# Kernel optimization log

Hardware: AMD Instinct MI355X
Metric: run time of the kernel (lower is better)

## Reference

```python
import jax, jax.numpy as jnp
import numpy as np

N_QUBITS = 4
N_LAYERS = 2


def _apply_rx(state, theta, wire):
    """Apply RX(theta) on `wire`. state: [B] + [2]*n complex. theta: [B] or scalar."""
    n = state.ndim - 1
    ax = wire + 1
    half = jnp.asarray(theta) * 0.5
    c = jnp.cos(half)
    s = jnp.sin(half)
    # broadcast angle over the remaining qubit axes after taking the wire slice
    c = jnp.reshape(c, c.shape + (1,) * (n - 1))
    s = jnp.reshape(s, s.shape + (1,) * (n - 1))
    s0 = jnp.take(state, 0, axis=ax)
    s1 = jnp.take(state, 1, axis=ax)
    new0 = c * s0 - 1j * s * s1
    new1 = -1j * s * s0 + c * s1
    return jnp.stack([new0, new1], axis=ax)


def _apply_cnot(state, control, target):
    cax = control + 1
    tax = target + 1
    sub0 = jnp.take(state, 0, axis=cax)
    sub1 = jnp.take(state, 1, axis=cax)
    tax_sub = tax if tax < cax else tax - 1
    sub1 = jnp.flip(sub1, axis=tax_sub)  # X on target when control == 1
    return jnp.stack([sub0, sub1], axis=cax)


def _quantum_circuit(x, w):
    """AngleEmbedding(RX) + BasicEntanglerLayers(RX + CNOT ring), PauliZ expvals.
    x: [B, n_qubits] float32 angles; w: [n_layers, n_qubits] float32.
    Returns [B, n_qubits] float32."""
    B = x.shape[0]
    n = N_QUBITS
    state = jnp.zeros((B,) + (2,) * n, dtype=jnp.complex64)
    state = state.at[(slice(None),) + (0,) * n].set(1.0)
    # AngleEmbedding: RX(x_q) on wire q (per-sample angles)
    for q in range(n):
        state = _apply_rx(state, x[:, q], q)
    # BasicEntanglerLayers: per layer, RX(w[l,q]) on each wire then CNOT ring
    for l in range(N_LAYERS):
        for q in range(n):
            state = _apply_rx(state, w[l, q], q)
        for q in range(n):
            state = _apply_cnot(state, q, (q + 1) % n)
    probs = jnp.abs(state) ** 2  # [B, 2,2,2,2]
    flat = probs.reshape(B, -1)  # [B, 16]
    # <Z_q> = sum_b p(b) * (+1 if bit q == 0 else -1)
    bits = ((jnp.arange(2 ** n)[:, None] >> (n - 1 - jnp.arange(n))[None, :]) & 1)
    signs = (1.0 - 2.0 * bits).astype(jnp.float32)  # [16, n]
    return flat @ signs  # [B, n]


def setup_inputs() -> dict:
    key = jax.random.key(0)
    ks = jax.random.split(key, 5)
    B = 65536
    inputs = jax.random.normal(ks[0], (B, 28, 28), dtype=jnp.float32)
    W1 = jax.random.normal(ks[1], (784, N_QUBITS), dtype=jnp.float32) * 0.05
    b1 = jnp.zeros((N_QUBITS,), dtype=jnp.float32)
    qw = jax.random.normal(ks[2], (N_LAYERS, N_QUBITS), dtype=jnp.float32) * 0.1
    W2 = jax.random.normal(ks[3], (N_QUBITS, 32), dtype=jnp.float32) * 0.3
    b2 = jnp.zeros((32,), dtype=jnp.float32)
    W3 = jax.random.normal(ks[4], (32, 2), dtype=jnp.float32) * 0.2
    b3 = jnp.zeros((2,), dtype=jnp.float32)
    return {"inputs": inputs, "W1": W1, "b1": b1, "qw": qw, "W2": W2, "b2": b2, "W3": W3, "b3": b3}


def reference(inputs, W1, b1, qw, W2, b2, W3, b3):
    B = inputs.shape[0]
    flat = inputs.reshape(B, -1)                      # flatten
    pre = jax.nn.relu(flat @ W1 + b1)                 # dense_preprocess [B, 4]
    q = _quantum_circuit(pre, qw)                     # [B, 4]
    q = jnp.where(jnp.isnan(q), jnp.zeros_like(q), q)
    post = jax.nn.relu(q @ W2 + b2)                   # dense_postprocess [B, 32]
    return jax.nn.softmax(post @ W3 + b3, axis=-1)    # output_layer [B, 2]
```

## Files before the change

### kernel.cpp

```cpp
#include <hip/hip_runtime.h>
#include <math.h>


constexpr int ROW   = 784;
constexpr int ROW4  = 196;
constexpr int CHS   = 20;

__global__ __launch_bounds__(256) void gemv_pre_kernel(
    const float* __restrict__ X,
    const float* __restrict__ W1,
    const float* __restrict__ b1,
    float* __restrict__ pre,
    int B)
{
    __shared__ float w_lds[ROW4 * CHS];

    for (int g = threadIdx.x; g < ROW; g += 256) {
        float4 v = reinterpret_cast<const float4*>(W1)[g];
        int chunk = g >> 2, part = g & 3;
        *reinterpret_cast<float4*>(&w_lds[chunk * CHS + part * 4]) = v;
    }
    const float bi0 = b1[0], bi1 = b1[1], bi2 = b1[2], bi3 = b1[3];
    __syncthreads();

    const int lane   = threadIdx.x & 63;
    const int waveG  = (blockIdx.x * 256 + threadIdx.x) >> 6;
    const int nWaves = (gridDim.x * 256) >> 6;

    for (int s = waveG; s < B; s += nWaves) {
        const float4* xrow = reinterpret_cast<const float4*>(X) + (size_t)s * ROW4;
        float a0 = 0.f, a1 = 0.f, a2 = 0.f, a3 = 0.f;
        for (int j4 = lane; j4 < ROW4; j4 += 64) {
            float4 x = xrow[j4];
            const float* wb = &w_lds[j4 * CHS];
            float4 w0 = *reinterpret_cast<const float4*>(wb + 0);
            float4 w1 = *reinterpret_cast<const float4*>(wb + 4);
            float4 w2 = *reinterpret_cast<const float4*>(wb + 8);
            float4 w3 = *reinterpret_cast<const float4*>(wb + 12);
            a0 = fmaf(x.x, w0.x, a0); a1 = fmaf(x.x, w0.y, a1);
            a2 = fmaf(x.x, w0.z, a2); a3 = fmaf(x.x, w0.w, a3);
            a0 = fmaf(x.y, w1.x, a0); a1 = fmaf(x.y, w1.y, a1);
            a2 = fmaf(x.y, w1.z, a2); a3 = fmaf(x.y, w1.w, a3);
            a0 = fmaf(x.z, w2.x, a0); a1 = fmaf(x.z, w2.y, a1);
            a2 = fmaf(x.z, w2.z, a2); a3 = fmaf(x.z, w2.w, a3);
            a0 = fmaf(x.w, w3.x, a0); a1 = fmaf(x.w, w3.y, a1);
            a2 = fmaf(x.w, w3.z, a2); a3 = fmaf(x.w, w3.w, a3);
        }
        #pragma unroll
        for (int off = 32; off > 0; off >>= 1) {
            a0 += __shfl_xor(a0, off);
            a1 += __shfl_xor(a1, off);
            a2 += __shfl_xor(a2, off);
            a3 += __shfl_xor(a3, off);
        }
        if (lane == 0) {
            float4 r;
            r.x = fmaxf(a0 + bi0, 0.f);
            r.y = fmaxf(a1 + bi1, 0.f);
            r.z = fmaxf(a2 + bi2, 0.f);
            r.w = fmaxf(a3 + bi3, 0.f);
            reinterpret_cast<float4*>(pre)[s] = r;
        }
    }
}


__device__ __forceinline__ void apply_rx(float (&sr)[16], float (&si)[16],
                                         int mask, float c, float s)
{
    #pragma unroll
    for (int i = 0; i < 16; i++) {
        if (!(i & mask)) {
            int j = i | mask;
            float x0 = sr[i], y0 = si[i], x1 = sr[j], y1 = si[j];
            sr[i] = fmaf(c, x0,  s * y1);
            si[i] = fmaf(c, y0, -s * x1);
            sr[j] = fmaf(c, x1,  s * y0);
            si[j] = fmaf(c, y1, -s * x0);
        }
    }
}

__device__ __forceinline__ void apply_cnot(float (&sr)[16], float (&si)[16],
                                           int cmask, int tmask)
{
    #pragma unroll
    for (int i = 0; i < 16; i++) {
        if ((i & cmask) && !(i & tmask)) {
            int j = i | tmask;
            float tr = sr[i]; sr[i] = sr[j]; sr[j] = tr;
            float ti = si[i]; si[i] = si[j]; si[j] = ti;
        }
    }
}

__global__ __launch_bounds__(256) void epilogue_kernel(
    const float* __restrict__ pre,
    const float* __restrict__ qw,
    const float* __restrict__ W2,
    const float* __restrict__ b2,
    const float* __restrict__ W3,
    const float* __restrict__ b3,
    float* __restrict__ out,
    int B)
{
    int s = blockIdx.x * blockDim.x + threadIdx.x;
    if (s >= B) return;

    float4 ang = reinterpret_cast<const float4*>(pre)[s];

    float sr[16], si[16];
    #pragma unroll
    for (int i = 0; i < 16; i++) { sr[i] = 0.f; si[i] = 0.f; }
    sr[0] = 1.f;

    {
        float c, sn;
        __sincosf(ang.x * 0.5f, &sn, &c); apply_rx(sr, si, 8, c, sn);
        __sincosf(ang.y * 0.5f, &sn, &c); apply_rx(sr, si, 4, c, sn);
        __sincosf(ang.z * 0.5f, &sn, &c); apply_rx(sr, si, 2, c, sn);
        __sincosf(ang.w * 0.5f, &sn, &c); apply_rx(sr, si, 1, c, sn);
    }

    #pragma unroll
    for (int l = 0; l < 2; l++) {
        #pragma unroll
        for (int q = 0; q < 4; q++) {
            float c, sn;
            __sincosf(qw[l * 4 + q] * 0.5f, &sn, &c);
            apply_rx(sr, si, 8 >> q, c, sn);
        }
        apply_cnot(sr, si, 8, 4);
        apply_cnot(sr, si, 4, 2);
        apply_cnot(sr, si, 2, 1);
        apply_cnot(sr, si, 1, 8);
    }

    float z0 = 0.f, z1 = 0.f, z2 = 0.f, z3 = 0.f;
    #pragma unroll
    for (int i = 0; i < 16; i++) {
        float p = fmaf(sr[i], sr[i], si[i] * si[i]);
        z0 += (i & 8) ? -p : p;
        z1 += (i & 4) ? -p : p;
        z2 += (i & 2) ? -p : p;
        z3 += (i & 1) ? -p : p;
    }
    z0 = (z0 == z0) ? z0 : 0.f;
    z1 = (z1 == z1) ? z1 : 0.f;
    z2 = (z2 == z2) ? z2 : 0.f;
    z3 = (z3 == z3) ? z3 : 0.f;

    float l0 = b3[0], l1 = b3[1];
    #pragma unroll
    for (int k = 0; k < 32; k++) {
        float v = b2[k];
        v = fmaf(z0, W2[k],      v);
        v = fmaf(z1, W2[32 + k], v);
        v = fmaf(z2, W2[64 + k], v);
        v = fmaf(z3, W2[96 + k], v);
        v = fmaxf(v, 0.f);
        l0 = fmaf(v, W3[2 * k],     l0);
        l1 = fmaf(v, W3[2 * k + 1], l1);
    }

    float m  = fmaxf(l0, l1);
    float e0 = __expf(l0 - m), e1 = __expf(l1 - m);
    float inv = 1.f / (e0 + e1);
    reinterpret_cast<float2*>(out)[s] = make_float2(e0 * inv, e1 * inv);
}

extern "C" void kernel_launch(void* const* d_in, const int* in_sizes, int n_in,
                              void* d_out, int out_size, void* d_ws, size_t ws_size,
                              hipStream_t stream)
{
    const float* X  = (const float*)d_in[0];
    const float* W1 = (const float*)d_in[1];
    const float* b1 = (const float*)d_in[2];
    const float* qw = (const float*)d_in[3];
    const float* W2 = (const float*)d_in[4];
    const float* b2 = (const float*)d_in[5];
    const float* W3 = (const float*)d_in[6];
    const float* b3 = (const float*)d_in[7];

    const int B = in_sizes[0] / ROW;
    float* pre = (float*)d_ws;

    gemv_pre_kernel<<<2048, 256, 0, stream>>>(X, W1, b1, pre, B);
    epilogue_kernel<<<(B + 255) / 256, 256, 0, stream>>>(pre, qw, W2, b2, W3, b3,
                                                         (float*)d_out, B);
}
```

Baseline: 296.6 us.

## Process four rows per wave with 16-lane groups and preloaded x registers

Each 64-lane wave now splits into four 16-lane groups, each reducing its own row, so all lanes stay busy (the old 196-float4 row left many lanes idle in the final iteration). All 13 float4 loads per lane are issued up front into registers to raise memory-level parallelism, the shuffle reduction is shortened to four steps, and launch bounds now request higher occupancy. This assumes B is a multiple of four (leftover rows would be dropped) and uses more registers.

```diff
diff --git a/kernel.cpp b/kernel.cpp
--- a/kernel.cpp
+++ b/kernel.cpp
@@ -6,7 +6,7 @@
 constexpr int ROW4  = 196;
 constexpr int CHS   = 20;
 
-__global__ __launch_bounds__(256) void gemv_pre_kernel(
+__global__ __launch_bounds__(256, 4) void gemv_pre_16lane_kernel(
     const float* __restrict__ X,
     const float* __restrict__ W1,
     const float* __restrict__ b1,
@@ -24,36 +24,48 @@
     __syncthreads();
 
     const int lane   = threadIdx.x & 63;
+    const int sub    = lane & 15;
+    const int grp    = lane >> 4;
     const int waveG  = (blockIdx.x * 256 + threadIdx.x) >> 6;
     const int nWaves = (gridDim.x * 256) >> 6;
-
-    for (int s = waveG; s < B; s += nWaves) {
+    const int nBatch = B >> 2;
+
+    for (int t = waveG; t < nBatch; t += nWaves) {
+        const int s = t * 4 + grp;
         const float4* xrow = reinterpret_cast<const float4*>(X) + (size_t)s * ROW4;
+
+        float4 x[13];
+        #pragma unroll
+        for (int i = 0; i < 12; i++) x[i] = xrow[sub + (i << 4)];
+        x[12] = (sub < 4) ? xrow[192 + sub] : make_float4(0.f, 0.f, 0.f, 0.f);
+
         float a0 = 0.f, a1 = 0.f, a2 = 0.f, a3 = 0.f;
-        for (int j4 = lane; j4 < ROW4; j4 += 64) {
-            float4 x = xrow[j4];
+        #pragma unroll
+        for (int i = 0; i < 13; i++) {
+            const int j4 = (i < 12) ? (sub + (i << 4)) : (192 + (sub & 3));
             const float* wb = &w_lds[j4 * CHS];
             float4 w0 = *reinterpret_cast<const float4*>(wb + 0);
             float4 w1 = *reinterpret_cast<const float4*>(wb + 4);
             float4 w2 = *reinterpret_cast<const float4*>(wb + 8);
             float4 w3 = *reinterpret_cast<const float4*>(wb + 12);
-            a0 = fmaf(x.x, w0.x, a0); a1 = fmaf(x.x, w0.y, a1);
-            a2 = fmaf(x.x, w0.z, a2); a3 = fmaf(x.x, w0.w, a3);
-            a0 = fmaf(x.y, w1.x, a0); a1 = fmaf(x.y, w1.y, a1);
-            a2 = fmaf(x.y, w1.z, a2); a3 = fmaf(x.y, w1.w, a3);
-            a0 = fmaf(x.z, w2.x, a0); a1 = fmaf(x.z, w2.y, a1);
-            a2 = fmaf(x.z, w2.z, a2); a3 = fmaf(x.z, w2.w, a3);
-            a0 = fmaf(x.w, w3.x, a0); a1 = fmaf(x.w, w3.y, a1);
-            a2 = fmaf(x.w, w3.z, a2); a3 = fmaf(x.w, w3.w, a3);
-        }
-        #pragma unroll
-        for (int off = 32; off > 0; off >>= 1) {
+            a0 = fmaf(x[i].x, w0.x, a0); a1 = fmaf(x[i].x, w0.y, a1);
+            a2 = fmaf(x[i].x, w0.z, a2); a3 = fmaf(x[i].x, w0.w, a3);
+            a0 = fmaf(x[i].y, w1.x, a0); a1 = fmaf(x[i].y, w1.y, a1);
+            a2 = fmaf(x[i].y, w1.z, a2); a3 = fmaf(x[i].y, w1.w, a3);
+            a0 = fmaf(x[i].z, w2.x, a0); a1 = fmaf(x[i].z, w2.y, a1);
+            a2 = fmaf(x[i].z, w2.z, a2); a3 = fmaf(x[i].z, w2.w, a3);
+            a0 = fmaf(x[i].w, w3.x, a0); a1 = fmaf(x[i].w, w3.y, a1);
+            a2 = fmaf(x[i].w, w3.z, a2); a3 = fmaf(x[i].w, w3.w, a3);
+        }
+
+        #pragma unroll
+        for (int off = 8; off > 0; off >>= 1) {
             a0 += __shfl_xor(a0, off);
             a1 += __shfl_xor(a1, off);
             a2 += __shfl_xor(a2, off);
             a3 += __shfl_xor(a3, off);
         }
-        if (lane == 0) {
+        if (sub == 0) {
             float4 r;
             r.x = fmaxf(a0 + bi0, 0.f);
             r.y = fmaxf(a1 + bi1, 0.f);
@@ -185,7 +197,7 @@
     const int B = in_sizes[0] / ROW;
     float* pre = (float*)d_ws;
 
-    gemv_pre_kernel<<<2048, 256, 0, stream>>>(X, W1, b1, pre, B);
+    gemv_pre_16lane_kernel<<<2048, 256, 0, stream>>>(X, W1, b1, pre, B);
     epilogue_kernel<<<(B + 255) / 256, 256, 0, stream>>>(pre, qw, W2, b2, W3, b3,
                                                          (float*)d_out, B);
 }
```

New measurement: 410.8 us. 38.5% more time.

## Fuse GEMV preprocess into quantum epilogue with one thread per sample

Applied to the files above, without the earlier changes.

Merges the wave-per-row GEMV kernel and the circuit/MLP epilogue into a single kernel in which each thread computes one sample's 784-long dot product, then runs the circuit directly. This removes the intermediate pre buffer, a second launch, and the cross-lane shuffle reductions, and adds register double-buffering of row loads. The trade-off is that each thread reads its own 3 KB row, so lanes of a wave access addresses strided by 3136 bytes and global loads are uncoalesced. The kernel relies on L2/cache-line reuse across iterations. LDS weight reads become broadcasts.

```diff
diff --git a/kernel.cpp b/kernel.cpp
--- a/kernel.cpp
+++ b/kernel.cpp
@@ -4,66 +4,6 @@
 
 constexpr int ROW   = 784;
 constexpr int ROW4  = 196;
-constexpr int CHS   = 20;
-
-__global__ __launch_bounds__(256) void gemv_pre_kernel(
-    const float* __restrict__ X,
-    const float* __restrict__ W1,
-    const float* __restrict__ b1,
-    float* __restrict__ pre,
-    int B)
-{
-    __shared__ float w_lds[ROW4 * CHS];
-
-    for (int g = threadIdx.x; g < ROW; g += 256) {
-        float4 v = reinterpret_cast<const float4*>(W1)[g];
-        int chunk = g >> 2, part = g & 3;
-        *reinterpret_cast<float4*>(&w_lds[chunk * CHS + part * 4]) = v;
-    }
-    const float bi0 = b1[0], bi1 = b1[1], bi2 = b1[2], bi3 = b1[3];
-    __syncthreads();
-
-    const int lane   = threadIdx.x & 63;
-    const int waveG  = (blockIdx.x * 256 + threadIdx.x) >> 6;
-    const int nWaves = (gridDim.x * 256) >> 6;
-
-    for (int s = waveG; s < B; s += nWaves) {
-        const float4* xrow = reinterpret_cast<const float4*>(X) + (size_t)s * ROW4;
-        float a0 = 0.f, a1 = 0.f, a2 = 0.f, a3 = 0.f;
-        for (int j4 = lane; j4 < ROW4; j4 += 64) {
-            float4 x = xrow[j4];
-            const float* wb = &w_lds[j4 * CHS];
-            float4 w0 = *reinterpret_cast<const float4*>(wb + 0);
-            float4 w1 = *reinterpret_cast<const float4*>(wb + 4);
-            float4 w2 = *reinterpret_cast<const float4*>(wb + 8);
-            float4 w3 = *reinterpret_cast<const float4*>(wb + 12);
-            a0 = fmaf(x.x, w0.x, a0); a1 = fmaf(x.x, w0.y, a1);
-            a2 = fmaf(x.x, w0.z, a2); a3 = fmaf(x.x, w0.w, a3);
-            a0 = fmaf(x.y, w1.x, a0); a1 = fmaf(x.y, w1.y, a1);
-            a2 = fmaf(x.y, w1.z, a2); a3 = fmaf(x.y, w1.w, a3);
-            a0 = fmaf(x.z, w2.x, a0); a1 = fmaf(x.z, w2.y, a1);
-            a2 = fmaf(x.z, w2.z, a2); a3 = fmaf(x.z, w2.w, a3);
-            a0 = fmaf(x.w, w3.x, a0); a1 = fmaf(x.w, w3.y, a1);
-            a2 = fmaf(x.w, w3.z, a2); a3 = fmaf(x.w, w3.w, a3);
-        }
-        #pragma unroll
-        for (int off = 32; off > 0; off >>= 1) {
-            a0 += __shfl_xor(a0, off);
-            a1 += __shfl_xor(a1, off);
-            a2 += __shfl_xor(a2, off);
-            a3 += __shfl_xor(a3, off);
-        }
-        if (lane == 0) {
-            float4 r;
-            r.x = fmaxf(a0 + bi0, 0.f);
-            r.y = fmaxf(a1 + bi1, 0.f);
-            r.z = fmaxf(a2 + bi2, 0.f);
-            r.w = fmaxf(a3 + bi3, 0.f);
-            reinterpret_cast<float4*>(pre)[s] = r;
-        }
-    }
-}
-
 
 __device__ __forceinline__ void apply_rx(float (&sr)[16], float (&si)[16],
                                          int mask, float c, float s)
@@ -94,8 +34,10 @@
     }
 }
 
-__global__ __launch_bounds__(256) void epilogue_kernel(
-    const float* __restrict__ pre,
+__global__ __launch_bounds__(256) void fused_model_kernel(
+    const float* __restrict__ X,
+    const float* __restrict__ W1,
+    const float* __restrict__ b1,
     const float* __restrict__ qw,
     const float* __restrict__ W2,
     const float* __restrict__ b2,
@@ -104,10 +46,53 @@
     float* __restrict__ out,
     int B)
 {
-    int s = blockIdx.x * blockDim.x + threadIdx.x;
+    __shared__ float4 w_lds[ROW];
+    const float4* W1f4 = reinterpret_cast<const float4*>(W1);
+    for (int g = threadIdx.x; g < ROW; g += 256) w_lds[g] = W1f4[g];
+    __syncthreads();
+
+    const int s = blockIdx.x * 256 + threadIdx.x;
     if (s >= B) return;
 
-    float4 ang = reinterpret_cast<const float4*>(pre)[s];
+    const float4* xr = reinterpret_cast<const float4*>(X) + (size_t)s * ROW4;
+
+    float a0 = 0.f, a1 = 0.f, a2 = 0.f, a3 = 0.f;
+
+    float4 A0 = xr[0], A1 = xr[1], A2 = xr[2], A3 = xr[3];
+    float4 B0 = xr[4], B1 = xr[5], B2 = xr[6], B3 = xr[7];
+
+    #pragma unroll 3
+    for (int c = 0; c < 49; c++) {
+        const int nx = (c < 47) ? ((c + 2) << 2) : 0;
+        float4 C0 = xr[nx], C1 = xr[nx + 1], C2 = xr[nx + 2], C3 = xr[nx + 3];
+
+        const float4* wl = &w_lds[c << 4];
+        float4 w;
+        w = wl[0];  a0=fmaf(A0.x,w.x,a0); a1=fmaf(A0.x,w.y,a1); a2=fmaf(A0.x,w.z,a2); a3=fmaf(A0.x,w.w,a3);
+        w = wl[1];  a0=fmaf(A0.y,w.x,a0); a1=fmaf(A0.y,w.y,a1); a2=fmaf(A0.y,w.z,a2); a3=fmaf(A0.y,w.w,a3);
+        w = wl[2];  a0=fmaf(A0.z,w.x,a0); a1=fmaf(A0.z,w.y,a1); a2=fmaf(A0.z,w.z,a2); a3=fmaf(A0.z,w.w,a3);
+        w = wl[3];  a0=fmaf(A0.w,w.x,a0); a1=fmaf(A0.w,w.y,a1); a2=fmaf(A0.w,w.z,a2); a3=fmaf(A0.w,w.w,a3);
+        w = wl[4];  a0=fmaf(A1.x,w.x,a0); a1=fmaf(A1.x,w.y,a1); a2=fmaf(A1.x,w.z,a2); a3=fmaf(A1.x,w.w,a3);
+        w = wl[5];  a0=fmaf(A1.y,w.x,a0); a1=fmaf(A1.y,w.y,a1); a2=fmaf(A1.y,w.z,a2); a3=fmaf(A1.y,w.w,a3);
+        w = wl[6];  a0=fmaf(A1.z,w.x,a0); a1=fmaf(A1.z,w.y,a1); a2=fmaf(A1.z,w.z,a2); a3=fmaf(A1.z,w.w,a3);
+        w = wl[7];  a0=fmaf(A1.w,w.x,a0); a1=fmaf(A1.w,w.y,a1); a2=fmaf(A1.w,w.z,a2); a3=fmaf(A1.w,w.w,a3);
+        w = wl[8];  a0=fmaf(A2.x,w.x,a0); a1=fmaf(A2.x,w.y,a1); a2=fmaf(A2.x,w.z,a2); a3=fmaf(A2.x,w.w,a3);
+        w = wl[9];  a0=fmaf(A2.y,w.x,a0); a1=fmaf(A2.y,w.y,a1); a2=fmaf(A2.y,w.z,a2); a3=fmaf(A2.y,w.w,a3);
+        w = wl[10]; a0=fmaf(A2.z,w.x,a0); a1=fmaf(A2.z,w.y,a1); a2=fmaf(A2.z,w.z,a2); a3=fmaf(A2.z,w.w,a3);
+        w = wl[11]; a0=fmaf(A2.w,w.x,a0); a1=fmaf(A2.w,w.y,a1); a2=fmaf(A2.w,w.z,a2); a3=fmaf(A2.w,w.w,a3);
+        w = wl[12]; a0=fmaf(A3.x,w.x,a0); a1=fmaf(A3.x,w.y,a1); a2=fmaf(A3.x,w.z,a2); a3=fmaf(A3.x,w.w,a3);
+        w = wl[13]; a0=fmaf(A3.y,w.x,a0); a1=fmaf(A3.y,w.y,a1); a2=fmaf(A3.y,w.z,a2); a3=fmaf(A3.y,w.w,a3);
+        w = wl[14]; a0=fmaf(A3.z,w.x,a0); a1=fmaf(A3.z,w.y,a1); a2=fmaf(A3.z,w.z,a2); a3=fmaf(A3.z,w.w,a3);
+        w = wl[15]; a0=fmaf(A3.w,w.x,a0); a1=fmaf(A3.w,w.y,a1); a2=fmaf(A3.w,w.z,a2); a3=fmaf(A3.w,w.w,a3);
+
+        A0 = B0; A1 = B1; A2 = B2; A3 = B3;
+        B0 = C0; B1 = C1; B2 = C2; B3 = C3;
+    }
+
+    const float ang0 = fmaxf(a0 + b1[0], 0.f);
+    const float ang1 = fmaxf(a1 + b1[1], 0.f);
+    const float ang2 = fmaxf(a2 + b1[2], 0.f);
+    const float ang3 = fmaxf(a3 + b1[3], 0.f);
 
     float sr[16], si[16];
     #pragma unroll
@@ -116,10 +101,10 @@
 
     {
         float c, sn;
-        __sincosf(ang.x * 0.5f, &sn, &c); apply_rx(sr, si, 8, c, sn);
-        __sincosf(ang.y * 0.5f, &sn, &c); apply_rx(sr, si, 4, c, sn);
-        __sincosf(ang.z * 0.5f, &sn, &c); apply_rx(sr, si, 2, c, sn);
-        __sincosf(ang.w * 0.5f, &sn, &c); apply_rx(sr, si, 1, c, sn);
+        __sincosf(ang0 * 0.5f, &sn, &c); apply_rx(sr, si, 8, c, sn);
+        __sincosf(ang1 * 0.5f, &sn, &c); apply_rx(sr, si, 4, c, sn);
+        __sincosf(ang2 * 0.5f, &sn, &c); apply_rx(sr, si, 2, c, sn);
+        __sincosf(ang3 * 0.5f, &sn, &c); apply_rx(sr, si, 1, c, sn);
     }
 
     #pragma unroll
@@ -183,9 +168,7 @@
     const float* b3 = (const float*)d_in[7];
 
     const int B = in_sizes[0] / ROW;
-    float* pre = (float*)d_ws;
 
-    gemv_pre_kernel<<<2048, 256, 0, stream>>>(X, W1, b1, pre, B);
-    epilogue_kernel<<<(B + 255) / 256, 256, 0, stream>>>(pre, qw, W2, b2, W3, b3,
-                                                         (float*)d_out, B);
+    fused_model_kernel<<<(B + 255) / 256, 256, 0, stream>>>(
+        X, W1, b1, qw, W2, b2, W3, b3, (float*)d_out, B);
 }
```

Result: no change. 299.2 us (+0.9%).
